# Kernel optimization log

Hardware: AMD Instinct MI355X
Metric: run time of the kernel (lower is better)

## Reference

```python
import jax, jax.numpy as jnp
import numpy as np

V = 1024          # vocab_size
N = 500_000       # num automaton states
A = 16            # arcs per non-start state (start state has V dense arcs)
MAX_ORDER = 4     # max n-gram order -> max backoff chain length
START = 0         # start (unigram) state
B = 8192          # batch of hypotheses


def _build_automaton(seed=0):
    rng = np.random.default_rng(seed)
    num_arcs = V + (N - 1) * A
    arcs_weights = -(rng.random(num_arcs).astype(np.float32) * 8.0 + 0.05)
    to_states = rng.integers(0, N, num_arcs).astype(np.int32)
    ilabels = np.empty(num_arcs, np.int32)
    ilabels[:V] = np.arange(V, dtype=np.int32)  # start state: arc index == ilabel
    # unique sorted ilabels per non-start state
    base = rng.integers(0, V, N - 1).astype(np.int32)
    offs = np.arange(A, dtype=np.int32) * (V // A)
    ilabels[V:] = np.sort((base[:, None] + offs[None, :]) % V, axis=1).reshape(-1)
    state_start = np.empty(N, np.int32)
    state_end = np.empty(N, np.int32)
    state_start[0] = 0
    state_end[0] = V
    state_start[1:] = V + np.arange(N - 1, dtype=np.int32) * A
    state_end[1:] = state_start[1:] + A
    # state orders: start=1, rest in 2..MAX_ORDER; backoff goes to an order-(k-1) state
    order = np.empty(N, np.int64)
    order[0] = 1
    order[1:] = rng.integers(2, MAX_ORDER + 1, N - 1)
    order[1:MAX_ORDER] = np.arange(2, MAX_ORDER + 1)  # guarantee each order nonempty
    backoff_to = np.zeros(N, np.int32)               # order-2 states back off to START
    for k in range(3, MAX_ORDER + 1):
        mask = order == k
        prev = np.flatnonzero(order == k - 1)
        backoff_to[mask] = rng.choice(prev, mask.sum()).astype(np.int32)
    backoff_weights = -(rng.random(N).astype(np.float32) * 3.0)
    backoff_weights[0] = 0.0
    return dict(
        arcs_weights=jnp.asarray(arcs_weights),
        backoff_weights=jnp.asarray(backoff_weights),
        ilabels=jnp.asarray(ilabels),
        to_states=jnp.asarray(to_states),
        backoff_to_states=jnp.asarray(backoff_to),
        state_start_arcs=jnp.asarray(state_start),
        state_end_arcs=jnp.asarray(state_end),
    )


def setup_inputs() -> dict:
    key = jax.random.key(0)
    inp = _build_automaton(0)
    inp["states"] = jax.random.randint(key, (B,), 0, N, dtype=jnp.int32)
    return inp


def _advance(states, arcs_weights, backoff_weights, ilabels, to_states,
             backoff_to_states, state_start_arcs, state_end_arcs):
    b = states.shape[0]
    rows = jnp.arange(b)[:, None]
    # column V is a dump slot for masked-out scatters
    scores_e = jnp.zeros((b, V + 1), arcs_weights.dtype)
    next_e = jnp.zeros((b, V + 1), jnp.int32)
    found_e = jnp.zeros((b, V + 1), bool)
    cur = states.astype(jnp.int32)
    acc = jnp.zeros((b,), arcs_weights.dtype)  # accumulated backoff weight
    offs = jnp.arange(A, dtype=jnp.int32)
    for _ in range(MAX_ORDER - 1):  # chase backoffs down to the start state
        at_start = cur == START
        idx = state_start_arcs[cur][:, None] + offs                    # [b, A]
        valid = (idx < state_end_arcs[cur][:, None]) & (~at_start)[:, None]
        idx = jnp.where(valid, idx, 0)
        lab = ilabels[idx]                                             # [b, A]
        can = valid & ~jnp.take_along_axis(found_e, lab, axis=1)
        slot = jnp.where(can, lab, V)
        scores_e = scores_e.at[rows, slot].set(acc[:, None] + arcs_weights[idx])
        next_e = next_e.at[rows, slot].set(to_states[idx])
        found_e = found_e.at[rows, slot].set(True)
        acc = jnp.where(at_start, acc, acc + backoff_weights[cur])
        cur = jnp.where(at_start, cur, backoff_to_states[cur])
    # start state has a dense arc table: arc index == ilabel for 0..V-1
    nf = ~found_e[:, :V]
    scores = jnp.where(nf, acc[:, None] + arcs_weights[None, :V], scores_e[:, :V])
    next_states = jnp.where(nf, to_states[None, :V], next_e[:, :V])
    return scores, next_states


def reference(states, arcs_weights, backoff_weights, ilabels, to_states,
              backoff_to_states, state_start_arcs, state_end_arcs):
    return _advance(states, arcs_weights, backoff_weights, ilabels, to_states,
                    backoff_to_states, state_start_arcs, state_end_arcs)
```

## Files before the change

### kernel.cpp

```cpp
#include <hip/hip_runtime.h>

#define VOCAB 1024
#define ARCS  16
#define MAX_ORDER 4
#define CHAIN (MAX_ORDER - 1)
#define START_STATE 0
#define WAVE 64

__global__ __launch_bounds__(WAVE, 8) void ngram_advance_kernel(
    const float* __restrict__ arcs_weights,
    const float* __restrict__ backoff_weights,
    const int*   __restrict__ ilabels,
    const int*   __restrict__ to_states,
    const int*   __restrict__ backoff_to,
    const int*   __restrict__ state_start,
    const int*   __restrict__ state_end,
    const int*   __restrict__ states,
    float*       __restrict__ out_scores,
    float*       __restrict__ out_next)
{
    const int tid = threadIdx.x;
    const int b   = blockIdx.x;

    int   cur = states[b];
    float acc = 0.0f;
    const int   cs0 = cur;  const float ca0 = acc;
    if (cur != START_STATE) { acc += backoff_weights[cur]; cur = backoff_to[cur]; }
    const int   cs1 = cur;  const float ca1 = acc;
    if (cur != START_STATE) { acc += backoff_weights[cur]; cur = backoff_to[cur]; }
    const int   cs2 = cur;  const float ca2 = acc;
    if (cur != START_STATE) { acc += backoff_weights[cur]; }
    const float accf = acc;

    const int level = tid >> 4;
    const int arc   = tid & (ARCS - 1);
    int   lab = -1, ns = 0;
    float sc  = 0.0f;
    bool  ok  = false;
    if (tid < CHAIN * ARCS) {
        const int   s    = (level == 0) ? cs0 : ((level == 1) ? cs1 : cs2);
        const float cacc = (level == 0) ? ca0 : ((level == 1) ? ca1 : ca2);
        if (s != START_STATE) {
            const int idx = state_start[s] + arc;
            if (idx < state_end[s]) {
                lab = ilabels[idx];
                sc  = cacc + arcs_weights[idx];
                ns  = to_states[idx];
                ok  = true;
            }
        }
    }

    int kill = 0;
    #pragma unroll
    for (int k = 0; k < 2 * ARCS; ++k) {
        const int lk = __builtin_amdgcn_readlane(lab, k);
        if (k < ARCS) kill |= (int)(level >= 1) & (int)(lab == lk);
        else          kill |= (int)(level == 2) & (int)(lab == lk);
    }
    const bool do_scatter = ok && !kill;

    float* __restrict__ so = out_scores + (size_t)b * VOCAB;
    float* __restrict__ no = out_next   + (size_t)b * VOCAB;
    #pragma unroll
    for (int i = 0; i < VOCAB / (WAVE * 4); ++i) {
        const int v = (tid + i * WAVE) * 4;
        const float4 dw = *(const float4*)&arcs_weights[v];
        const int4   dn = *(const int4*)&to_states[v];
        float4 rs, rn;
        rs.x = accf + dw.x;  rs.y = accf + dw.y;
        rs.z = accf + dw.z;  rs.w = accf + dw.w;
        rn.x = (float)dn.x;  rn.y = (float)dn.y;
        rn.z = (float)dn.z;  rn.w = (float)dn.w;
        *(float4*)&so[v] = rs;
        *(float4*)&no[v] = rn;
    }

    asm volatile("s_waitcnt vmcnt(0)" ::: "memory");

    if (do_scatter) {
        so[lab] = sc;
        no[lab] = (float)ns;
    }
}

extern "C" void kernel_launch(void* const* d_in, const int* in_sizes, int n_in,
                              void* d_out, int out_size, void* d_ws, size_t ws_size,
                              hipStream_t stream) {
    const float* arcs_weights    = (const float*)d_in[0];
    const float* backoff_weights = (const float*)d_in[1];
    const int*   ilabels         = (const int*)d_in[2];
    const int*   to_states       = (const int*)d_in[3];
    const int*   backoff_to      = (const int*)d_in[4];
    const int*   state_start     = (const int*)d_in[5];
    const int*   state_end       = (const int*)d_in[6];
    const int*   states          = (const int*)d_in[7];

    const int B = in_sizes[7];
    float* out_scores = (float*)d_out;
    float* out_next   = out_scores + (size_t)B * VOCAB;

    ngram_advance_kernel<<<B, WAVE, 0, stream>>>(
        arcs_weights, backoff_weights, ilabels, to_states, backoff_to,
        state_start, state_end, states, out_scores, out_next);
}
```

Before: 20.11 us.

## Pack four hypotheses per block, hoist next-state stores, use nontemporal stores

Each block now handles four hypotheses, one per wavefront, instead of one hypothesis per 64-thread block, which cuts the block count. The dense next-state table is written before the backoff-chain loads, so those dependent loads overlap with the stores. The dense score writes are placed after the arc gathers, and all dense writes now use nontemporal stores to reduce cache pollution. The launch assumes B is divisible by four, and the per-wave pointer math relies on readfirstlane.

```diff
diff --git a/kernel.cpp b/kernel.cpp
--- a/kernel.cpp
+++ b/kernel.cpp
@@ -6,8 +6,13 @@
 #define CHAIN (MAX_ORDER - 1)
 #define START_STATE 0
 #define WAVE 64
+#define HYP_PER_BLOCK 4
+#define BLOCK (WAVE * HYP_PER_BLOCK)
 
-__global__ __launch_bounds__(WAVE, 8) void ngram_advance_kernel(
+typedef float f32x4 __attribute__((ext_vector_type(4)));
+typedef int   i32x4 __attribute__((ext_vector_type(4)));
+
+__global__ __launch_bounds__(BLOCK, 8) void ngram_advance_kernel(
     const float* __restrict__ arcs_weights,
     const float* __restrict__ backoff_weights,
     const int*   __restrict__ ilabels,
@@ -19,10 +24,25 @@
     float*       __restrict__ out_scores,
     float*       __restrict__ out_next)
 {
-    const int tid = threadIdx.x;
-    const int b   = blockIdx.x;
+    const int lane = threadIdx.x & (WAVE - 1);
+    const int b = __builtin_amdgcn_readfirstlane(
+        blockIdx.x * HYP_PER_BLOCK + (threadIdx.x >> 6));
 
-    int   cur = states[b];
+    int cur = states[b];
+
+    float* __restrict__ so = out_scores + (size_t)b * VOCAB;
+    float* __restrict__ no = out_next   + (size_t)b * VOCAB;
+
+    #pragma unroll
+    for (int i = 0; i < VOCAB / (WAVE * 4); ++i) {
+        const int v = (lane + i * WAVE) * 4;
+        const i32x4 dn = *(const i32x4*)&to_states[v];
+        f32x4 rn;
+        rn.x = (float)dn.x;  rn.y = (float)dn.y;
+        rn.z = (float)dn.z;  rn.w = (float)dn.w;
+        __builtin_nontemporal_store(rn, (f32x4*)&no[v]);
+    }
+
     float acc = 0.0f;
     const int   cs0 = cur;  const float ca0 = acc;
     if (cur != START_STATE) { acc += backoff_weights[cur]; cur = backoff_to[cur]; }
@@ -32,12 +52,12 @@
     if (cur != START_STATE) { acc += backoff_weights[cur]; }
     const float accf = acc;
 
-    const int level = tid >> 4;
-    const int arc   = tid & (ARCS - 1);
+    const int level = lane >> 4;
+    const int arc   = lane & (ARCS - 1);
     int   lab = -1, ns = 0;
     float sc  = 0.0f;
     bool  ok  = false;
-    if (tid < CHAIN * ARCS) {
+    if (lane < CHAIN * ARCS) {
         const int   s    = (level == 0) ? cs0 : ((level == 1) ? cs1 : cs2);
         const float cacc = (level == 0) ? ca0 : ((level == 1) ? ca1 : ca2);
         if (s != START_STATE) {
@@ -51,6 +71,16 @@
         }
     }
 
+    #pragma unroll
+    for (int i = 0; i < VOCAB / (WAVE * 4); ++i) {
+        const int v = (lane + i * WAVE) * 4;
+        const f32x4 dw = *(const f32x4*)&arcs_weights[v];
+        f32x4 rs;
+        rs.x = accf + dw.x;  rs.y = accf + dw.y;
+        rs.z = accf + dw.z;  rs.w = accf + dw.w;
+        __builtin_nontemporal_store(rs, (f32x4*)&so[v]);
+    }
+
     int kill = 0;
     #pragma unroll
     for (int k = 0; k < 2 * ARCS; ++k) {
@@ -59,22 +89,6 @@
         else          kill |= (int)(level == 2) & (int)(lab == lk);
     }
     const bool do_scatter = ok && !kill;
-
-    float* __restrict__ so = out_scores + (size_t)b * VOCAB;
-    float* __restrict__ no = out_next   + (size_t)b * VOCAB;
-    #pragma unroll
-    for (int i = 0; i < VOCAB / (WAVE * 4); ++i) {
-        const int v = (tid + i * WAVE) * 4;
-        const float4 dw = *(const float4*)&arcs_weights[v];
-        const int4   dn = *(const int4*)&to_states[v];
-        float4 rs, rn;
-        rs.x = accf + dw.x;  rs.y = accf + dw.y;
-        rs.z = accf + dw.z;  rs.w = accf + dw.w;
-        rn.x = (float)dn.x;  rn.y = (float)dn.y;
-        rn.z = (float)dn.z;  rn.w = (float)dn.w;
-        *(float4*)&so[v] = rs;
-        *(float4*)&no[v] = rn;
-    }
 
     asm volatile("s_waitcnt vmcnt(0)" ::: "memory");
 
@@ -100,7 +114,7 @@
     float* out_scores = (float*)d_out;
     float* out_next   = out_scores + (size_t)B * VOCAB;
 
-    ngram_advance_kernel<<<B, WAVE, 0, stream>>>(
+    ngram_advance_kernel<<<B / HYP_PER_BLOCK, BLOCK, 0, stream>>>(
         arcs_weights, backoff_weights, ilabels, to_states, backoff_to,
         state_start, state_end, states, out_scores, out_next);
 }
```

Result: slower. 27.07 us (+34.6%).
